# Kernel tuning notes

Measured on AMD Instinct MI355X. Metric: run time of the kernel, lower is better.

## Reference

```python
import jax, jax.numpy as jnp
import numpy as np

B, C_IN, C_OUT, K, H, W_DIM, F_IN = 16, 64, 64, 3, 128, 128, 16
NKW = C_OUT * C_IN * K * K  # 36864 kernel weights per sample


def setup_inputs() -> dict:
    key = jax.random.key(0)
    ks = jax.random.split(key, 8)
    s = 0.05
    return {
        "x": jax.random.normal(ks[0], (B, C_IN, H, W_DIM), dtype=jnp.float32),
        "z": jax.random.normal(ks[1], (B, F_IN), dtype=jnp.float32),
        "W0": jax.random.normal(ks[2], (20, F_IN), dtype=jnp.float32) * s,
        "b0": jax.random.normal(ks[3], (20,), dtype=jnp.float32) * s,
        "W1": jax.random.normal(ks[4], (30, 20), dtype=jnp.float32) * s,
        "b1": jax.random.normal(ks[5], (30,), dtype=jnp.float32) * s,
        "W2": jax.random.normal(ks[6], (NKW + C_OUT, 30), dtype=jnp.float32) * s,
        "b2": jax.random.normal(ks[7], (NKW + C_OUT,), dtype=jnp.float32) * s,
    }


def reference(x, z, W0, b0, W1, b1, W2, b2):
    # Manifold MLP: ReLU after EVERY layer, including the final one (as in original code).
    h = jax.nn.relu(z @ W0.T + b0)
    h = jax.nn.relu(h @ W1.T + b1)
    aw = jax.nn.relu(h @ W2.T + b2)  # [B, NKW + C_OUT]

    kernels = aw[:, :NKW].reshape(B, C_OUT, C_IN, K, K)  # per-sample OIHW kernels
    biases = aw[:, NKW:]  # [B, C_OUT]

    def conv_one(xi, wi, bi):
        # xi: [C_IN, H, W], wi: [C_OUT, C_IN, K, K], bi: [C_OUT]
        y = jax.lax.conv_general_dilated(
            xi[None], wi, window_strides=(1, 1), padding="SAME",
            dimension_numbers=("NCHW", "OIHW", "NCHW"))[0]
        return y + bi[:, None, None]

    out = jax.vmap(conv_one)(x, kernels, biases)  # [B, C_OUT, H, W]
    return jax.nn.relu(out)
```

## Files before the change

### kernel.cpp

```cpp
#include <hip/hip_runtime.h>


typedef __bf16 bf16;
typedef __bf16 bf16x8 __attribute__((ext_vector_type(8)));
typedef float f32x4 __attribute__((ext_vector_type(4)));

#define NB 16
#define CI 64
#define CO 64
#define HH 128
#define WW 128
#define TS 16
#define HALO 18
#define CPAD 72
#define WPAD 72
#define NKW 36864
#define NROWS 36928

__global__ __launch_bounds__(256)
void hyper_kernel(const float* __restrict__ z, const float* __restrict__ W0,
                  const float* __restrict__ b0, const float* __restrict__ W1,
                  const float* __restrict__ b1, const float* __restrict__ W2,
                  const float* __restrict__ b2, bf16* __restrict__ wt,
                  float* __restrict__ biases) {
  __shared__ float h1s[NB][30];
  const int tid = threadIdx.x;
  if (tid < NB) {
    float h0[20];
    #pragma unroll
    for (int i = 0; i < 20; ++i) {
      float s = b0[i];
      #pragma unroll
      for (int j = 0; j < 16; ++j) s += W0[i * 16 + j] * z[tid * 16 + j];
      h0[i] = fmaxf(s, 0.f);
    }
    #pragma unroll
    for (int i = 0; i < 30; ++i) {
      float s = b1[i];
      #pragma unroll
      for (int j = 0; j < 20; ++j) s += W1[i * 20 + j] * h0[j];
      h1s[tid][i] = fmaxf(s, 0.f);
    }
  }
  __syncthreads();
  const int r = blockIdx.x * 256 + tid;
  if (r >= NROWS) return;
  float w2r[30];
  #pragma unroll
  for (int j = 0; j < 30; ++j) w2r[j] = W2[r * 30 + j];
  const float bb = b2[r];
  const bool isk = r < NKW;
  int co = 0, ci = 0, tap = 0;
  if (isk) {
    co = r / 576;
    int rem = r - co * 576;
    ci = rem / 9;
    tap = rem - ci * 9;
  }
  for (int b = 0; b < NB; ++b) {
    float s = bb;
    #pragma unroll
    for (int j = 0; j < 30; ++j) s += w2r[j] * h1s[b][j];
    s = fmaxf(s, 0.f);
    if (isk)
      wt[((size_t)((b * 9 + tap) * CO + co)) * CI + ci] = (bf16)s;
    else
      biases[b * CO + (r - NKW)] = s;
  }
}

__global__ __launch_bounds__(1024)
void conv_kernel(const float* __restrict__ x, const bf16* __restrict__ wt,
                 const float* __restrict__ bias, float* __restrict__ out) {
  __shared__ __align__(16) bf16 xt[HALO * HALO * CPAD];
  __shared__ __align__(16) bf16 wts[CO * WPAD];

  const int b = blockIdx.z;
  const int x0 = blockIdx.x * TS;
  const int y0 = blockIdx.y * TS;
  const int tid = threadIdx.x;

  for (int e = tid; e < HALO * HALO * CI; e += 1024) {
    int ci = e / (HALO * HALO);
    int p = e - ci * (HALO * HALO);
    int py = p / HALO;
    int px = p - py * HALO;
    int gy = y0 + py - 1, gx = x0 + px - 1;
    float v = 0.f;
    if (gy >= 0 && gy < HH && gx >= 0 && gx < WW)
      v = x[((size_t)(b * CI + ci) * HH + gy) * WW + gx];
    xt[(py * HALO + px) * CPAD + ci] = (bf16)v;
  }

  const int lane = tid & 63;
  const int wv = tid >> 6;
  const int m = lane & 15;
  const int q = lane >> 4;
  const int cg0 = (wv & 1) * 2;
  const int ty0 = (wv >> 1) * 2;

  f32x4 acc[2][2];
  #pragma unroll
  for (int i = 0; i < 2; ++i)
    #pragma unroll
    for (int j = 0; j < 2; ++j) acc[i][j] = (f32x4){0.f, 0.f, 0.f, 0.f};

  const int wco = tid >> 4;
  const int wci = (tid & 15) * 4;
  const bf16* wsrc = wt + (size_t)b * 9 * CO * CI + (size_t)wco * CI + wci;

  for (int tap = 0; tap < 9; ++tap) {
    __syncthreads();
    *reinterpret_cast<uint2*>(&wts[wco * WPAD + wci]) =
        *reinterpret_cast<const uint2*>(wsrc + (size_t)tap * CO * CI);
    __syncthreads();
    const int dy = tap / 3, dx = tap - dy * 3;
    #pragma unroll
    for (int kh = 0; kh < 2; ++kh) {
      const int ci0 = kh * 32 + q * 8;
      bf16x8 a0 = *reinterpret_cast<const bf16x8*>(
          &wts[(cg0 * 16 + m) * WPAD + ci0]);
      bf16x8 a1 = *reinterpret_cast<const bf16x8*>(
          &wts[((cg0 + 1) * 16 + m) * WPAD + ci0]);
      bf16x8 bv0 = *reinterpret_cast<const bf16x8*>(
          &xt[((ty0 + dy) * HALO + (m + dx)) * CPAD + ci0]);
      bf16x8 bv1 = *reinterpret_cast<const bf16x8*>(
          &xt[((ty0 + 1 + dy) * HALO + (m + dx)) * CPAD + ci0]);
      acc[0][0] = __builtin_amdgcn_mfma_f32_16x16x32_bf16(a0, bv0, acc[0][0], 0, 0, 0);
      acc[0][1] = __builtin_amdgcn_mfma_f32_16x16x32_bf16(a0, bv1, acc[0][1], 0, 0, 0);
      acc[1][0] = __builtin_amdgcn_mfma_f32_16x16x32_bf16(a1, bv0, acc[1][0], 0, 0, 0);
      acc[1][1] = __builtin_amdgcn_mfma_f32_16x16x32_bf16(a1, bv1, acc[1][1], 0, 0, 0);
    }
  }

  #pragma unroll
  for (int i = 0; i < 2; ++i) {
    #pragma unroll
    for (int j = 0; j < 2; ++j) {
      const int gy = y0 + ty0 + j;
      #pragma unroll
      for (int r = 0; r < 4; ++r) {
        const int co = (cg0 + i) * 16 + q * 4 + r;
        float v = acc[i][j][r] + bias[b * CO + co];
        out[((size_t)(b * CO + co) * HH + gy) * WW + x0 + m] = fmaxf(v, 0.f);
      }
    }
  }
}

extern "C" void kernel_launch(void* const* d_in, const int* in_sizes, int n_in,
                              void* d_out, int out_size, void* d_ws,
                              size_t ws_size, hipStream_t stream) {
  const float* x = (const float*)d_in[0];
  const float* z = (const float*)d_in[1];
  const float* W0 = (const float*)d_in[2];
  const float* b0 = (const float*)d_in[3];
  const float* W1 = (const float*)d_in[4];
  const float* b1 = (const float*)d_in[5];
  const float* W2 = (const float*)d_in[6];
  const float* b2 = (const float*)d_in[7];
  float* out = (float*)d_out;

  bf16* wt = (bf16*)d_ws;
  float* biases = (float*)((char*)d_ws + (size_t)NB * 9 * CO * CI * 2);

  hipLaunchKernelGGL(hyper_kernel, dim3((NROWS + 255) / 256), dim3(256), 0,
                     stream, z, W0, b0, W1, b1, W2, b2, wt, biases);
  hipLaunchKernelGGL(conv_kernel, dim3(WW / TS, HH / TS, NB), dim3(1024), 0,
                     stream, x, wt, biases, out);
}
```

Baseline: 184.0 us.

## Keep conv weights in registers, enlarge per-wave tile, coalesce weight generation writes

The hypernetwork kernel now assigns threads by output layout (tap, co, ci), so the bf16 weight writes are contiguous. The bias rows get their own block. The conv kernel drops the shared weight staging and its two barriers per tap. Each wave instead loads its A fragments straight from global memory into registers, prefetching the next tap, and computes an 8-row by 16-channel tile with 512 threads per block. The halo load packs 8 channels per thread into one vector LDS store. The trade-off is more accumulator registers and repeated weight reads from global or L2 by each wave.

```diff
diff --git a/kernel.cpp b/kernel.cpp
--- a/kernel.cpp
+++ b/kernel.cpp
@@ -13,7 +13,6 @@
 #define TS 16
 #define HALO 18
 #define CPAD 72
-#define WPAD 72
 #define NKW 36864
 #define NROWS 36928
 
@@ -43,107 +42,118 @@
     }
   }
   __syncthreads();
-  const int r = blockIdx.x * 256 + tid;
-  if (r >= NROWS) return;
-  float w2r[30];
-  #pragma unroll
-  for (int j = 0; j < 30; ++j) w2r[j] = W2[r * 30 + j];
-  const float bb = b2[r];
-  const bool isk = r < NKW;
-  int co = 0, ci = 0, tap = 0;
-  if (isk) {
-    co = r / 576;
-    int rem = r - co * 576;
-    ci = rem / 9;
-    tap = rem - ci * 9;
-  }
-  for (int b = 0; b < NB; ++b) {
-    float s = bb;
+
+  if (blockIdx.x < 144) {
+    const int e = blockIdx.x * 256 + tid;
+    const int tap = e >> 12;
+    const int rem = e & 4095;
+    const int co = rem >> 6;
+    const int ci = rem & 63;
+    const int r = co * 576 + ci * 9 + tap;
+    float w2r[30];
     #pragma unroll
-    for (int j = 0; j < 30; ++j) s += w2r[j] * h1s[b][j];
-    s = fmaxf(s, 0.f);
-    if (isk)
-      wt[((size_t)((b * 9 + tap) * CO + co)) * CI + ci] = (bf16)s;
-    else
-      biases[b * CO + (r - NKW)] = s;
+    for (int j = 0; j < 30; ++j) w2r[j] = W2[r * 30 + j];
+    const float bb = b2[r];
+    for (int b = 0; b < NB; ++b) {
+      float s = bb;
+      #pragma unroll
+      for (int j = 0; j < 30; ++j) s += w2r[j] * h1s[b][j];
+      wt[(size_t)b * NKW + e] = (bf16)fmaxf(s, 0.f);
+    }
+  } else {
+    if (tid < CO) {
+      const int r = NKW + tid;
+      float w2r[30];
+      #pragma unroll
+      for (int j = 0; j < 30; ++j) w2r[j] = W2[r * 30 + j];
+      const float bb = b2[r];
+      for (int b = 0; b < NB; ++b) {
+        float s = bb;
+        #pragma unroll
+        for (int j = 0; j < 30; ++j) s += w2r[j] * h1s[b][j];
+        biases[b * CO + tid] = fmaxf(s, 0.f);
+      }
+    }
   }
 }
 
-__global__ __launch_bounds__(1024)
+__global__ __launch_bounds__(512, 4)
 void conv_kernel(const float* __restrict__ x, const bf16* __restrict__ wt,
                  const float* __restrict__ bias, float* __restrict__ out) {
   __shared__ __align__(16) bf16 xt[HALO * HALO * CPAD];
-  __shared__ __align__(16) bf16 wts[CO * WPAD];
 
   const int b = blockIdx.z;
   const int x0 = blockIdx.x * TS;
   const int y0 = blockIdx.y * TS;
   const int tid = threadIdx.x;
 
-  for (int e = tid; e < HALO * HALO * CI; e += 1024) {
-    int ci = e / (HALO * HALO);
-    int p = e - ci * (HALO * HALO);
-    int py = p / HALO;
-    int px = p - py * HALO;
-    int gy = y0 + py - 1, gx = x0 + px - 1;
-    float v = 0.f;
-    if (gy >= 0 && gy < HH && gx >= 0 && gx < WW)
-      v = x[((size_t)(b * CI + ci) * HH + gy) * WW + gx];
-    xt[(py * HALO + px) * CPAD + ci] = (bf16)v;
+  for (int i = tid; i < 8 * HALO * HALO; i += 512) {
+    const int k = i / (HALO * HALO);
+    const int p = i - k * (HALO * HALO);
+    const int py = p / HALO;
+    const int px = p - py * HALO;
+    const int gy = y0 + py - 1, gx = x0 + px - 1;
+    bf16x8 v = {};
+    if (gy >= 0 && gy < HH && gx >= 0 && gx < WW) {
+      const float* xs = x + ((size_t)(b * CI + k * 8) * HH + gy) * WW + gx;
+      #pragma unroll
+      for (int j = 0; j < 8; ++j) v[j] = (bf16)xs[(size_t)j * HH * WW];
+    }
+    *reinterpret_cast<bf16x8*>(&xt[p * CPAD + k * 8]) = v;
   }
 
   const int lane = tid & 63;
   const int wv = tid >> 6;
   const int m = lane & 15;
   const int q = lane >> 4;
-  const int cg0 = (wv & 1) * 2;
-  const int ty0 = (wv >> 1) * 2;
+  const int cg = wv & 3;
+  const int ty0 = (wv >> 2) * 8;
 
-  f32x4 acc[2][2];
+  f32x4 acc[8];
   #pragma unroll
-  for (int i = 0; i < 2; ++i)
+  for (int r = 0; r < 8; ++r) acc[r] = (f32x4){0.f, 0.f, 0.f, 0.f};
+
+  const bf16* wbase =
+      wt + (size_t)b * 9 * CO * CI + (size_t)(cg * 16 + m) * CI + q * 8;
+
+  bf16x8 a_cur0 = *reinterpret_cast<const bf16x8*>(wbase);
+  bf16x8 a_cur1 = *reinterpret_cast<const bf16x8*>(wbase + 32);
+
+  __syncthreads();
+
+  #pragma unroll
+  for (int tap = 0; tap < 9; ++tap) {
+    bf16x8 a_n0 = a_cur0, a_n1 = a_cur1;
+    if (tap < 8) {
+      a_n0 = *reinterpret_cast<const bf16x8*>(wbase + (tap + 1) * CO * CI);
+      a_n1 = *reinterpret_cast<const bf16x8*>(wbase + (tap + 1) * CO * CI + 32);
+    }
+    const int dy = tap / 3, dx = tap - dy * 3;
+    const int pcol = m + dx;
     #pragma unroll
-    for (int j = 0; j < 2; ++j) acc[i][j] = (f32x4){0.f, 0.f, 0.f, 0.f};
-
-  const int wco = tid >> 4;
-  const int wci = (tid & 15) * 4;
-  const bf16* wsrc = wt + (size_t)b * 9 * CO * CI + (size_t)wco * CI + wci;
-
-  for (int tap = 0; tap < 9; ++tap) {
-    __syncthreads();
-    *reinterpret_cast<uint2*>(&wts[wco * WPAD + wci]) =
-        *reinterpret_cast<const uint2*>(wsrc + (size_t)tap * CO * CI);
-    __syncthreads();
-    const int dy = tap / 3, dx = tap - dy * 3;
+    for (int r = 0; r < 8; ++r) {
+      const int p = (ty0 + r + dy) * HALO + pcol;
+      bf16x8 bv0 = *reinterpret_cast<const bf16x8*>(&xt[p * CPAD + q * 8]);
+      acc[r] = __builtin_amdgcn_mfma_f32_16x16x32_bf16(a_cur0, bv0, acc[r], 0, 0, 0);
+    }
     #pragma unroll
-    for (int kh = 0; kh < 2; ++kh) {
-      const int ci0 = kh * 32 + q * 8;
-      bf16x8 a0 = *reinterpret_cast<const bf16x8*>(
-          &wts[(cg0 * 16 + m) * WPAD + ci0]);
-      bf16x8 a1 = *reinterpret_cast<const bf16x8*>(
-          &wts[((cg0 + 1) * 16 + m) * WPAD + ci0]);
-      bf16x8 bv0 = *reinterpret_cast<const bf16x8*>(
-          &xt[((ty0 + dy) * HALO + (m + dx)) * CPAD + ci0]);
-      bf16x8 bv1 = *reinterpret_cast<const bf16x8*>(
-          &xt[((ty0 + 1 + dy) * HALO + (m + dx)) * CPAD + ci0]);
-      acc[0][0] = __builtin_amdgcn_mfma_f32_16x16x32_bf16(a0, bv0, acc[0][0], 0, 0, 0);
-      acc[0][1] = __builtin_amdgcn_mfma_f32_16x16x32_bf16(a0, bv1, acc[0][1], 0, 0, 0);
-      acc[1][0] = __builtin_amdgcn_mfma_f32_16x16x32_bf16(a1, bv0, acc[1][0], 0, 0, 0);
-      acc[1][1] = __builtin_amdgcn_mfma_f32_16x16x32_bf16(a1, bv1, acc[1][1], 0, 0, 0);
+    for (int r = 0; r < 8; ++r) {
+      const int p = (ty0 + r + dy) * HALO + pcol;
+      bf16x8 bv1 = *reinterpret_cast<const bf16x8*>(&xt[p * CPAD + 32 + q * 8]);
+      acc[r] = __builtin_amdgcn_mfma_f32_16x16x32_bf16(a_cur1, bv1, acc[r], 0, 0, 0);
     }
+    a_cur0 = a_n0;
+    a_cur1 = a_n1;
   }
 
   #pragma unroll
-  for (int i = 0; i < 2; ++i) {
+  for (int r = 0; r < 8; ++r) {
+    const int gy = y0 + ty0 + r;
     #pragma unroll
-    for (int j = 0; j < 2; ++j) {
-      const int gy = y0 + ty0 + j;
-      #pragma unroll
-      for (int r = 0; r < 4; ++r) {
-        const int co = (cg0 + i) * 16 + q * 4 + r;
-        float v = acc[i][j][r] + bias[b * CO + co];
-        out[((size_t)(b * CO + co) * HH + gy) * WW + x0 + m] = fmaxf(v, 0.f);
-      }
+    for (int rg = 0; rg < 4; ++rg) {
+      const int co = cg * 16 + q * 4 + rg;
+      float v = acc[r][rg] + bias[b * CO + co];
+      out[((size_t)(b * CO + co) * HH + gy) * WW + x0 + m] = fmaxf(v, 0.f);
     }
   }
 }
@@ -164,8 +174,8 @@
   bf16* wt = (bf16*)d_ws;
   float* biases = (float*)((char*)d_ws + (size_t)NB * 9 * CO * CI * 2);
 
-  hipLaunchKernelGGL(hyper_kernel, dim3((NROWS + 255) / 256), dim3(256), 0,
-                     stream, z, W0, b0, W1, b1, W2, b2, wt, biases);
-  hipLaunchKernelGGL(conv_kernel, dim3(WW / TS, HH / TS, NB), dim3(1024), 0,
+  hipLaunchKernelGGL(hyper_kernel, dim3(145), dim3(256), 0, stream,
+                     z, W0, b0, W1, b1, W2, b2, wt, biases);
+  hipLaunchKernelGGL(conv_kernel, dim3(WW / TS, HH / TS, NB), dim3(512), 0,
                      stream, x, wt, biases, out);
 }
```

Result: slower. 322.9 us (+75.4%).
